# Optimization experiments

Hardware: AMD Instinct MI355X
Metric: run time of the kernel (lower is better)

## Reference

```python
import jax, jax.numpy as jnp
import numpy as np

N, K, D = 16384, 16, 16
TWO_PI = 2.0 * np.pi


def setup_inputs() -> dict:
    key = jax.random.key(0)
    k1, k2, k3, k4 = jax.random.split(key, 4)
    X = jax.random.normal(k1, (N, D), dtype=jnp.float32)
    mu = jax.random.normal(k2, (K, D), dtype=jnp.float32)
    L = jax.random.normal(k3, (K, D, D), dtype=jnp.float32)
    weights = jax.random.uniform(k4, (K,), dtype=jnp.float32)
    return {"X": X, "mu": mu, "L": L, "weights": weights, "it": 0}


def reference(X, mu, L, weights, it):
    # Covariance matrices A_k = tril(L_k) @ tril(L_k)^T + I  -> [K, D, D]
    Tl = jnp.tril(L)
    A = jnp.einsum('kab,kcb->kac', Tl, Tl) + jnp.eye(D, dtype=L.dtype)
    Sigma = jnp.linalg.inv(A)                                  # [K, D, D]

    # Gaussian product for all pairs (i, j):
    #   S_ij = inv(Sigma_i + Sigma_j), m_ij = S_ij (Sigma_i mu_i + Sigma_j mu_j)
    Ssum = Sigma[:, None] + Sigma[None, :]                     # [K, K, D, D]
    S = jnp.linalg.inv(Ssum)                                   # [K, K, D, D]
    rhs = jnp.einsum('kab,kb->ka', Sigma, mu)                  # Sigma_k mu_k
    m = jnp.einsum('ijab,ijb->ija', S, rhs[:, None] + rhs[None, :])  # [K, K, D]

    # Normalizer of the product Gaussian: z_ij = ((2pi)^D det(S_ij))^(-1/2)
    z = 1.0 / jnp.sqrt((TWO_PI ** D) * jnp.linalg.det(S))      # [K, K]
    P = jnp.linalg.inv(S)                                      # precision, [K, K, D, D]

    # Pair coefficient _product_z(i, j) (uses A as covariance here, as in source)
    Asum = A[:, None] + A[None, :]                             # [K, K, D, D]
    dmu = mu[:, None] - mu[None, :]                            # [K, K, D]
    q_mu = jnp.einsum('ijd,ijde,ije->ij', dmu, jnp.linalg.inv(Asum), dmu)
    pz = jnp.exp(-0.5 * q_mu) / jnp.sqrt(jnp.linalg.det(TWO_PI * Asum))

    # Mahalanobis distance of every sample to every pair mean: [N, K, K]
    diff = X[:, None, None, :] - m[None]                       # [N, K, K, D]
    quad = jnp.einsum('nijd,ijde,nije->nij', diff, P, diff)

    coef = pz * z * (weights[:, None] * weights[None, :])      # [K, K]
    pdf = jnp.einsum('ij,nij->n', coef, jnp.exp(-0.5 * quad))  # [N]
    return jnp.mean(jnp.log(pdf))
```

## Files before the change

kernel.cpp:

```cpp
#include <hip/hip_runtime.h>
#include <math.h>

#define NTOT 16384
#define KK 16
#define DD 16
#define NPAIR 136

#define WS_RHS   0
#define WS_WP    1024
#define WS_LCS   9792
#define WS_SIG   10336
#define WS_AF    26720
#define WS_PART  10336
#define WS_END   43104

#define LN2PI 1.8378770664093454836f

__global__ __launch_bounds__(256) void gm_pre(const float* __restrict__ mu,
                                              const float* __restrict__ L,
                                              char* __restrict__ wsb) {
  const int tid = threadIdx.x;
  const int k = tid >> 4;
  const int r = tid & 15;

  const float* Lk = L + k * DD * DD;
  float Lx[DD];
  #pragma unroll
  for (int b = 0; b < DD; b++) Lx[b] = (b <= r) ? Lk[r * DD + b] : 0.0f;

  float Ar[DD];
  #pragma unroll
  for (int c = 0; c < DD; c++) {
    float s = (r == c) ? 1.0f : 0.0f;
    #pragma unroll
    for (int b = 0; b <= c; b++)
      s = fmaf(Lx[b], __shfl(Lx[b], c, 16), s);
    Ar[c] = s;
  }
  {
    float* Aout = (float*)(wsb + WS_AF) + k * DD * DD;
    #pragma unroll
    for (int c = 0; c < DD; c++) Aout[r * DD + c] = Ar[c];
  }

  float Gr[DD];
  #pragma unroll
  for (int m = 0; m < DD; m++) Gr[m] = 0.0f;
  #pragma unroll
  for (int c = 0; c < DD; c++) {
    float u = Ar[c];
    #pragma unroll
    for (int m = 0; m < c; m++)
      u = fmaf(-Gr[m], __shfl(Gr[m], c, 16), u);
    float d = sqrtf(__shfl(u, c, 16));
    float val = (r == c) ? d : u / d;
    if (r >= c) Gr[c] = val;
  }

  float Wc[DD];
  #pragma unroll
  for (int m = 0; m < DD; m++) Wc[m] = 0.0f;
  #pragma unroll
  for (int rr = 0; rr < DD; rr++) {
    float s = (r == rr) ? 1.0f : 0.0f;
    #pragma unroll
    for (int m = 0; m < rr; m++)
      s = fmaf(-__shfl(Gr[m], rr, 16), Wc[m], s);
    Wc[rr] = s / __shfl(Gr[rr], rr, 16);
  }
  {
    float* Wout = (float*)(wsb + WS_WP) + k * 137;
    #pragma unroll
    for (int rr = 0; rr < DD; rr++)
      if (rr >= r) Wout[rr * (rr + 1) / 2 + r] = Wc[rr];
  }

  float Sig[DD];
  #pragma unroll
  for (int b = 0; b < DD; b++) {
    float s = 0.0f;
    #pragma unroll
    for (int rr = 0; rr < DD; rr++)
      s = fmaf(Wc[rr], __shfl(Wc[rr], b, 16), s);
    Sig[b] = s;
  }
  {
    float* Sout = (float*)(wsb + WS_SIG) + k * DD * DD;
    #pragma unroll
    for (int b = 0; b < DD; b++) Sout[r * DD + b] = Sig[b];
  }

  {
    float muv = mu[k * DD + r];
    float s = 0.0f;
    #pragma unroll
    for (int b = 0; b < DD; b++)
      s = fmaf(Sig[b], __shfl(muv, b, 16), s);
    ((float*)(wsb + WS_RHS))[k * DD + r] = s;
  }
}

__global__ __launch_bounds__(256) void gm_pair(const float* __restrict__ mu,
                                               const float* __restrict__ wts,
                                               char* __restrict__ wsb) {
  const int tid = threadIdx.x;
  const int g = (blockIdx.x << 4) + (tid >> 4);
  const int r = tid & 15;
  if (g >= NPAIR) return;
  int i = 0, rem = g;
  while (rem >= (KK - i)) { rem -= (KK - i); i++; }
  const int j = i + rem;

  const float* Sf = (const float*)(wsb + WS_SIG);
  const float* Af = (const float*)(wsb + WS_AF);
  const float* Rf = (const float*)(wsb + WS_RHS);

  float Mr[DD], Gr[DD];

  #pragma unroll
  for (int c = 0; c < DD; c++)
    Mr[c] = Sf[i * 256 + r * DD + c] + Sf[j * 256 + r * DD + c];

  float ldS = 0.0f, mydinv = 0.0f;
  #pragma unroll
  for (int m = 0; m < DD; m++) Gr[m] = 0.0f;
  #pragma unroll
  for (int c = 0; c < DD; c++) {
    float u = Mr[c];
    #pragma unroll
    for (int m = 0; m < c; m++)
      u = fmaf(-Gr[m], __shfl(Gr[m], c, 16), u);
    float d2 = __shfl(u, c, 16);
    ldS += __logf(d2);
    float d = sqrtf(d2);
    float dinv = 1.0f / d;
    if (r == c) mydinv = dinv;
    float val = (r == c) ? d : u * dinv;
    if (r >= c) Gr[c] = val;
  }
  float cq = 0.0f;
  {
    float acc = Rf[i * DD + r] + Rf[j * DD + r];
    #pragma unroll
    for (int m = 0; m < DD; m++) {
      float ym = __shfl(acc, m, 16) * __shfl(mydinv, m, 16);
      cq = fmaf(ym, ym, cq);
      if (r > m) acc = fmaf(-Gr[m], ym, acc);
    }
  }

  #pragma unroll
  for (int c = 0; c < DD; c++)
    Mr[c] = Af[i * 256 + r * DD + c] + Af[j * 256 + r * DD + c];

  float ldA = 0.0f, mydinvA = 0.0f;
  #pragma unroll
  for (int m = 0; m < DD; m++) Gr[m] = 0.0f;
  #pragma unroll
  for (int c = 0; c < DD; c++) {
    float u = Mr[c];
    #pragma unroll
    for (int m = 0; m < c; m++)
      u = fmaf(-Gr[m], __shfl(Gr[m], c, 16), u);
    float d2 = __shfl(u, c, 16);
    ldA += __logf(d2);
    float d = sqrtf(d2);
    float dinv = 1.0f / d;
    if (r == c) mydinvA = dinv;
    float val = (r == c) ? d : u * dinv;
    if (r >= c) Gr[c] = val;
  }
  float q = 0.0f;
  {
    float acc = mu[i * DD + r] - mu[j * DD + r];
    #pragma unroll
    for (int m = 0; m < DD; m++) {
      float ym = __shfl(acc, m, 16) * __shfl(mydinvA, m, 16);
      q = fmaf(ym, ym, q);
      if (r > m) acc = fmaf(-Gr[m], ym, acc);
    }
  }

  if (r == 0) {
    float lC = -0.5f * q - 0.5f * ldA + 0.5f * ldS - (float)DD * LN2PI
               + __logf(wts[i]) + __logf(wts[j]) - 0.5f * cq;
    if (i < j) lC += 0.69314718056f;
    ((float*)(wsb + WS_LCS))[g] = lC;
  }
}

__global__ __launch_bounds__(256) void gm_main(const float* __restrict__ X,
                                               char* __restrict__ wsb) {
  __shared__ float sW[KK * 137];
  __shared__ float sR[KK * 17];
  __shared__ float sLC[NPAIR];
  __shared__ unsigned char sIJ[NPAIR];
  __shared__ float sX[256];
  __shared__ float sE[16 * 17];
  __shared__ double sD[16];

  const int tid = threadIdx.x;
  const int s = tid >> 4;
  const int r = tid & 15;

  {
    const float* Wp = (const float*)(wsb + WS_WP);
    for (int idx = tid; idx < KK * 137; idx += 256) sW[idx] = Wp[idx];
    const float* Rf = (const float*)(wsb + WS_RHS);
    if (tid < 256) sR[(tid >> 4) * 17 + (tid & 15)] = Rf[tid];
    const float* lc = (const float*)(wsb + WS_LCS);
    if (tid < NPAIR) {
      sLC[tid] = lc[tid];
      int i = 0, rem = tid;
      while (rem >= (KK - i)) { rem -= (KK - i); i++; }
      sIJ[tid] = (unsigned char)((i << 4) | (i + rem));
    }
    if (tid < 64)
      ((float4*)sX)[tid] = ((const float4*)(X + (size_t)blockIdx.x * 256))[tid];
  }
  __syncthreads();

  float x[DD];
  {
    float4 b0 = ((const float4*)sX)[s * 4 + 0];
    float4 b1 = ((const float4*)sX)[s * 4 + 1];
    float4 b2 = ((const float4*)sX)[s * 4 + 2];
    float4 b3 = ((const float4*)sX)[s * 4 + 3];
    x[0]=b0.x; x[1]=b0.y; x[2]=b0.z; x[3]=b0.w;
    x[4]=b1.x; x[5]=b1.y; x[6]=b1.z; x[7]=b1.w;
    x[8]=b2.x; x[9]=b2.y; x[10]=b2.z; x[11]=b2.w;
    x[12]=b3.x; x[13]=b3.y; x[14]=b3.z; x[15]=b3.w;
  }

  {
    const float* Wk = &sW[r * 137];
    float g = 0.0f;
    #pragma unroll
    for (int rr = 0; rr < DD; rr++) {
      float y = 0.0f;
      #pragma unroll
      for (int c = 0; c <= rr; c++) y = fmaf(Wk[rr * (rr + 1) / 2 + c], x[c], y);
      g = fmaf(y, y, g);
    }
    float h = 0.0f;
    #pragma unroll
    for (int d = 0; d < DD; d++) h = fmaf(sR[r * 17 + d], x[d], h);
    sE[s * 17 + r] = fmaf(-0.5f, g, h);
  }
  __syncthreads();

  float val[9];
  float T = -3.0e38f;
  #pragma unroll
  for (int t = 0; t < 9; t++) {
    int p = t * 16 + r;
    if (t < 8 || r < 8) {
      int ij = sIJ[p];
      val[t] = sLC[p] + sE[s * 17 + (ij >> 4)] + sE[s * 17 + (ij & 15)];
    } else {
      val[t] = -3.0e38f;
    }
    T = fmaxf(T, val[t]);
  }
  #pragma unroll
  for (int w = 1; w < 16; w <<= 1) T = fmaxf(T, __shfl_xor(T, w, 16));

  float sum = 0.0f;
  #pragma unroll
  for (int t = 0; t < 9; t++) sum += __expf(val[t] - T);
  #pragma unroll
  for (int w = 1; w < 16; w <<= 1) sum += __shfl_xor(sum, w, 16);

  if (r == 0) sD[s] = (double)(T + __logf(sum));
  __syncthreads();
  if (tid == 0) {
    double acc = 0.0;
    #pragma unroll
    for (int m = 0; m < 16; m++) acc += sD[m];
    ((double*)(wsb + WS_PART))[blockIdx.x] = acc;
  }
}

__global__ __launch_bounds__(256) void gm_fin(const double* __restrict__ part,
                                              float* __restrict__ out) {
  int t = threadIdx.x;
  double v = part[t] + part[t + 256] + part[t + 512] + part[t + 768];
  #pragma unroll
  for (int off = 32; off > 0; off >>= 1) v += __shfl_down(v, off);
  __shared__ double r4[4];
  if ((t & 63) == 0) r4[t >> 6] = v;
  __syncthreads();
  if (t == 0) out[0] = (float)((r4[0] + r4[1] + r4[2] + r4[3]) * (1.0 / 16384.0));
}

extern "C" void kernel_launch(void* const* d_in, const int* in_sizes, int n_in,
                              void* d_out, int out_size, void* d_ws, size_t ws_size,
                              hipStream_t stream) {
  const float* X   = (const float*)d_in[0];
  const float* mu  = (const float*)d_in[1];
  const float* L   = (const float*)d_in[2];
  const float* wts = (const float*)d_in[3];
  char* wsb = (char*)d_ws;
  if (ws_size < WS_END) return;

  hipLaunchKernelGGL(gm_pre,  dim3(1), dim3(256), 0, stream, mu, L, wsb);
  hipLaunchKernelGGL(gm_pair, dim3(9), dim3(256), 0, stream, mu, wts, wsb);
  hipLaunchKernelGGL(gm_main, dim3(NTOT / 16), dim3(256), 0, stream, X, wsb);
  hipLaunchKernelGGL(gm_fin,  dim3(1), dim3(256), 0, stream,
                     (const double*)(wsb + WS_PART), (float*)d_out);
}
```

Baseline: 38.07 us.

## Fuse per-component and pair prep kernels, merge final reduction via atomics

Merges the per-component setup and pair-coefficient kernels into one 1024-thread block that keeps Sigma, A and rhs in shared memory instead of round-tripping through global workspace. The main kernel now processes two 256-sample tiles per block and performs the final reduction with a fixed-point 64-bit atomic accumulator plus a last-block counter, removing the separate finish kernel. This cuts the launch count from four to two. In exchange, the pair work runs on a single block, and the fixed-point conversion slightly quantizes the sum.

```diff
diff --git a/kernel.cpp b/kernel.cpp
--- a/kernel.cpp
+++ b/kernel.cpp
@@ -9,188 +9,190 @@
 #define WS_RHS   0
 #define WS_WP    1024
 #define WS_LCS   9792
-#define WS_SIG   10336
-#define WS_AF    26720
-#define WS_PART  10336
-#define WS_END   43104
+#define WS_ACC   10336
+#define WS_CNT   10344
+#define WS_END   10352
 
 #define LN2PI 1.8378770664093454836f
-
-__global__ __launch_bounds__(256) void gm_pre(const float* __restrict__ mu,
-                                              const float* __restrict__ L,
-                                              char* __restrict__ wsb) {
+#define FXSCALE 268435456.0
+
+__global__ __launch_bounds__(1024) void gm_prep(const float* __restrict__ mu,
+                                                const float* __restrict__ L,
+                                                const float* __restrict__ wts,
+                                                char* __restrict__ wsb) {
+  __shared__ float sSig[KK * 256];
+  __shared__ float sA[KK * 256];
+  __shared__ float sR[256];
+
   const int tid = threadIdx.x;
-  const int k = tid >> 4;
+  if (tid == 0) {
+    *(unsigned long long*)(wsb + WS_ACC) = 0ULL;
+    *(unsigned long long*)(wsb + WS_CNT) = 0ULL;
+  }
+
+  if (tid < 256) {
+    const int k = tid >> 4;
+    const int r = tid & 15;
+
+    const float* Lk = L + k * DD * DD;
+    float Lx[DD];
+    #pragma unroll
+    for (int b = 0; b < DD; b++) Lx[b] = (b <= r) ? Lk[r * DD + b] : 0.0f;
+
+    float Ar[DD];
+    #pragma unroll
+    for (int c = 0; c < DD; c++) {
+      float s = (r == c) ? 1.0f : 0.0f;
+      #pragma unroll
+      for (int b = 0; b <= c; b++)
+        s = fmaf(Lx[b], __shfl(Lx[b], c, 16), s);
+      Ar[c] = s;
+      sA[k * 256 + r * DD + c] = s;
+    }
+
+    float Gr[DD];
+    #pragma unroll
+    for (int m = 0; m < DD; m++) Gr[m] = 0.0f;
+    #pragma unroll
+    for (int c = 0; c < DD; c++) {
+      float u = Ar[c];
+      #pragma unroll
+      for (int m = 0; m < c; m++)
+        u = fmaf(-Gr[m], __shfl(Gr[m], c, 16), u);
+      float d = sqrtf(__shfl(u, c, 16));
+      float val = (r == c) ? d : u / d;
+      if (r >= c) Gr[c] = val;
+    }
+
+    float Wc[DD];
+    #pragma unroll
+    for (int m = 0; m < DD; m++) Wc[m] = 0.0f;
+    #pragma unroll
+    for (int rr = 0; rr < DD; rr++) {
+      float s = (r == rr) ? 1.0f : 0.0f;
+      #pragma unroll
+      for (int m = 0; m < rr; m++)
+        s = fmaf(-__shfl(Gr[m], rr, 16), Wc[m], s);
+      Wc[rr] = s / __shfl(Gr[rr], rr, 16);
+    }
+    {
+      float* Wout = (float*)(wsb + WS_WP) + k * 137;
+      #pragma unroll
+      for (int rr = 0; rr < DD; rr++)
+        if (rr >= r) Wout[rr * (rr + 1) / 2 + r] = Wc[rr];
+    }
+
+    float Sig[DD];
+    #pragma unroll
+    for (int b = 0; b < DD; b++) {
+      float s = 0.0f;
+      #pragma unroll
+      for (int rr = 0; rr < DD; rr++)
+        s = fmaf(Wc[rr], __shfl(Wc[rr], b, 16), s);
+      Sig[b] = s;
+      sSig[k * 256 + r * DD + b] = s;
+    }
+
+    {
+      float muv = mu[k * DD + r];
+      float s = 0.0f;
+      #pragma unroll
+      for (int b = 0; b < DD; b++)
+        s = fmaf(Sig[b], __shfl(muv, b, 16), s);
+      sR[k * DD + r] = s;
+      ((float*)(wsb + WS_RHS))[k * DD + r] = s;
+    }
+  }
+  __syncthreads();
+
+  const int g2 = tid >> 4;
   const int r = tid & 15;
 
-  const float* Lk = L + k * DD * DD;
-  float Lx[DD];
-  #pragma unroll
-  for (int b = 0; b < DD; b++) Lx[b] = (b <= r) ? Lk[r * DD + b] : 0.0f;
-
-  float Ar[DD];
-  #pragma unroll
-  for (int c = 0; c < DD; c++) {
-    float s = (r == c) ? 1.0f : 0.0f;
-    #pragma unroll
-    for (int b = 0; b <= c; b++)
-      s = fmaf(Lx[b], __shfl(Lx[b], c, 16), s);
-    Ar[c] = s;
-  }
-  {
-    float* Aout = (float*)(wsb + WS_AF) + k * DD * DD;
-    #pragma unroll
-    for (int c = 0; c < DD; c++) Aout[r * DD + c] = Ar[c];
-  }
-
-  float Gr[DD];
-  #pragma unroll
-  for (int m = 0; m < DD; m++) Gr[m] = 0.0f;
-  #pragma unroll
-  for (int c = 0; c < DD; c++) {
-    float u = Ar[c];
-    #pragma unroll
-    for (int m = 0; m < c; m++)
-      u = fmaf(-Gr[m], __shfl(Gr[m], c, 16), u);
-    float d = sqrtf(__shfl(u, c, 16));
-    float val = (r == c) ? d : u / d;
-    if (r >= c) Gr[c] = val;
-  }
-
-  float Wc[DD];
-  #pragma unroll
-  for (int m = 0; m < DD; m++) Wc[m] = 0.0f;
-  #pragma unroll
-  for (int rr = 0; rr < DD; rr++) {
-    float s = (r == rr) ? 1.0f : 0.0f;
-    #pragma unroll
-    for (int m = 0; m < rr; m++)
-      s = fmaf(-__shfl(Gr[m], rr, 16), Wc[m], s);
-    Wc[rr] = s / __shfl(Gr[rr], rr, 16);
-  }
-  {
-    float* Wout = (float*)(wsb + WS_WP) + k * 137;
-    #pragma unroll
-    for (int rr = 0; rr < DD; rr++)
-      if (rr >= r) Wout[rr * (rr + 1) / 2 + r] = Wc[rr];
-  }
-
-  float Sig[DD];
-  #pragma unroll
-  for (int b = 0; b < DD; b++) {
-    float s = 0.0f;
-    #pragma unroll
-    for (int rr = 0; rr < DD; rr++)
-      s = fmaf(Wc[rr], __shfl(Wc[rr], b, 16), s);
-    Sig[b] = s;
-  }
-  {
-    float* Sout = (float*)(wsb + WS_SIG) + k * DD * DD;
-    #pragma unroll
-    for (int b = 0; b < DD; b++) Sout[r * DD + b] = Sig[b];
-  }
-
-  {
-    float muv = mu[k * DD + r];
-    float s = 0.0f;
-    #pragma unroll
-    for (int b = 0; b < DD; b++)
-      s = fmaf(Sig[b], __shfl(muv, b, 16), s);
-    ((float*)(wsb + WS_RHS))[k * DD + r] = s;
+  for (int t = 0; t < 3; t++) {
+    const int p = g2 + (t << 6);
+    if (p >= NPAIR) break;
+    int i = 0, rem = p;
+    while (rem >= (KK - i)) { rem -= (KK - i); i++; }
+    const int j = i + rem;
+
+    float Mr[DD], Gr[DD];
+
+    #pragma unroll
+    for (int c = 0; c < DD; c++)
+      Mr[c] = sSig[i * 256 + r * DD + c] + sSig[j * 256 + r * DD + c];
+
+    float ldS = 0.0f, mydinv = 0.0f;
+    #pragma unroll
+    for (int m = 0; m < DD; m++) Gr[m] = 0.0f;
+    #pragma unroll
+    for (int c = 0; c < DD; c++) {
+      float u = Mr[c];
+      #pragma unroll
+      for (int m = 0; m < c; m++)
+        u = fmaf(-Gr[m], __shfl(Gr[m], c, 16), u);
+      float d2 = __shfl(u, c, 16);
+      ldS += __logf(d2);
+      float d = sqrtf(d2);
+      float dinv = 1.0f / d;
+      if (r == c) mydinv = dinv;
+      float val = (r == c) ? d : u * dinv;
+      if (r >= c) Gr[c] = val;
+    }
+    float cq = 0.0f;
+    {
+      float acc = sR[i * DD + r] + sR[j * DD + r];
+      #pragma unroll
+      for (int m = 0; m < DD; m++) {
+        float ym = __shfl(acc, m, 16) * __shfl(mydinv, m, 16);
+        cq = fmaf(ym, ym, cq);
+        if (r > m) acc = fmaf(-Gr[m], ym, acc);
+      }
+    }
+
+    #pragma unroll
+    for (int c = 0; c < DD; c++)
+      Mr[c] = sA[i * 256 + r * DD + c] + sA[j * 256 + r * DD + c];
+
+    float ldA = 0.0f, mydinvA = 0.0f;
+    #pragma unroll
+    for (int m = 0; m < DD; m++) Gr[m] = 0.0f;
+    #pragma unroll
+    for (int c = 0; c < DD; c++) {
+      float u = Mr[c];
+      #pragma unroll
+      for (int m = 0; m < c; m++)
+        u = fmaf(-Gr[m], __shfl(Gr[m], c, 16), u);
+      float d2 = __shfl(u, c, 16);
+      ldA += __logf(d2);
+      float d = sqrtf(d2);
+      float dinv = 1.0f / d;
+      if (r == c) mydinvA = dinv;
+      float val = (r == c) ? d : u * dinv;
+      if (r >= c) Gr[c] = val;
+    }
+    float q = 0.0f;
+    {
+      float acc = mu[i * DD + r] - mu[j * DD + r];
+      #pragma unroll
+      for (int m = 0; m < DD; m++) {
+        float ym = __shfl(acc, m, 16) * __shfl(mydinvA, m, 16);
+        q = fmaf(ym, ym, q);
+        if (r > m) acc = fmaf(-Gr[m], ym, acc);
+      }
+    }
+
+    if (r == 0) {
+      float lC = -0.5f * q - 0.5f * ldA + 0.5f * ldS - (float)DD * LN2PI
+                 + __logf(wts[i]) + __logf(wts[j]) - 0.5f * cq;
+      if (i < j) lC += 0.69314718056f;
+      ((float*)(wsb + WS_LCS))[p] = lC;
+    }
   }
 }
 
-__global__ __launch_bounds__(256) void gm_pair(const float* __restrict__ mu,
-                                               const float* __restrict__ wts,
-                                               char* __restrict__ wsb) {
-  const int tid = threadIdx.x;
-  const int g = (blockIdx.x << 4) + (tid >> 4);
-  const int r = tid & 15;
-  if (g >= NPAIR) return;
-  int i = 0, rem = g;
-  while (rem >= (KK - i)) { rem -= (KK - i); i++; }
-  const int j = i + rem;
-
-  const float* Sf = (const float*)(wsb + WS_SIG);
-  const float* Af = (const float*)(wsb + WS_AF);
-  const float* Rf = (const float*)(wsb + WS_RHS);
-
-  float Mr[DD], Gr[DD];
-
-  #pragma unroll
-  for (int c = 0; c < DD; c++)
-    Mr[c] = Sf[i * 256 + r * DD + c] + Sf[j * 256 + r * DD + c];
-
-  float ldS = 0.0f, mydinv = 0.0f;
-  #pragma unroll
-  for (int m = 0; m < DD; m++) Gr[m] = 0.0f;
-  #pragma unroll
-  for (int c = 0; c < DD; c++) {
-    float u = Mr[c];
-    #pragma unroll
-    for (int m = 0; m < c; m++)
-      u = fmaf(-Gr[m], __shfl(Gr[m], c, 16), u);
-    float d2 = __shfl(u, c, 16);
-    ldS += __logf(d2);
-    float d = sqrtf(d2);
-    float dinv = 1.0f / d;
-    if (r == c) mydinv = dinv;
-    float val = (r == c) ? d : u * dinv;
-    if (r >= c) Gr[c] = val;
-  }
-  float cq = 0.0f;
-  {
-    float acc = Rf[i * DD + r] + Rf[j * DD + r];
-    #pragma unroll
-    for (int m = 0; m < DD; m++) {
-      float ym = __shfl(acc, m, 16) * __shfl(mydinv, m, 16);
-      cq = fmaf(ym, ym, cq);
-      if (r > m) acc = fmaf(-Gr[m], ym, acc);
-    }
-  }
-
-  #pragma unroll
-  for (int c = 0; c < DD; c++)
-    Mr[c] = Af[i * 256 + r * DD + c] + Af[j * 256 + r * DD + c];
-
-  float ldA = 0.0f, mydinvA = 0.0f;
-  #pragma unroll
-  for (int m = 0; m < DD; m++) Gr[m] = 0.0f;
-  #pragma unroll
-  for (int c = 0; c < DD; c++) {
-    float u = Mr[c];
-    #pragma unroll
-    for (int m = 0; m < c; m++)
-      u = fmaf(-Gr[m], __shfl(Gr[m], c, 16), u);
-    float d2 = __shfl(u, c, 16);
-    ldA += __logf(d2);
-    float d = sqrtf(d2);
-    float dinv = 1.0f / d;
-    if (r == c) mydinvA = dinv;
-    float val = (r == c) ? d : u * dinv;
-    if (r >= c) Gr[c] = val;
-  }
-  float q = 0.0f;
-  {
-    float acc = mu[i * DD + r] - mu[j * DD + r];
-    #pragma unroll
-    for (int m = 0; m < DD; m++) {
-      float ym = __shfl(acc, m, 16) * __shfl(mydinvA, m, 16);
-      q = fmaf(ym, ym, q);
-      if (r > m) acc = fmaf(-Gr[m], ym, acc);
-    }
-  }
-
-  if (r == 0) {
-    float lC = -0.5f * q - 0.5f * ldA + 0.5f * ldS - (float)DD * LN2PI
-               + __logf(wts[i]) + __logf(wts[j]) - 0.5f * cq;
-    if (i < j) lC += 0.69314718056f;
-    ((float*)(wsb + WS_LCS))[g] = lC;
-  }
-}
-
-__global__ __launch_bounds__(256) void gm_main(const float* __restrict__ X,
-                                               char* __restrict__ wsb) {
+__global__ __launch_bounds__(256) void gm_all(const float* __restrict__ X,
+                                              char* __restrict__ wsb,
+                                              float* __restrict__ out) {
   __shared__ float sW[KK * 137];
   __shared__ float sR[KK * 17];
   __shared__ float sLC[NPAIR];
@@ -207,7 +209,7 @@
     const float* Wp = (const float*)(wsb + WS_WP);
     for (int idx = tid; idx < KK * 137; idx += 256) sW[idx] = Wp[idx];
     const float* Rf = (const float*)(wsb + WS_RHS);
-    if (tid < 256) sR[(tid >> 4) * 17 + (tid & 15)] = Rf[tid];
+    sR[s * 17 + r] = Rf[tid];
     const float* lc = (const float*)(wsb + WS_LCS);
     if (tid < NPAIR) {
       sLC[tid] = lc[tid];
@@ -215,82 +217,93 @@
       while (rem >= (KK - i)) { rem -= (KK - i); i++; }
       sIJ[tid] = (unsigned char)((i << 4) | (i + rem));
     }
+  }
+
+  double blockAcc = 0.0;
+
+  #pragma unroll
+  for (int tile = 0; tile < 2; tile++) {
+    __syncthreads();
     if (tid < 64)
-      ((float4*)sX)[tid] = ((const float4*)(X + (size_t)blockIdx.x * 256))[tid];
-  }
-  __syncthreads();
-
-  float x[DD];
-  {
-    float4 b0 = ((const float4*)sX)[s * 4 + 0];
-    float4 b1 = ((const float4*)sX)[s * 4 + 1];
-    float4 b2 = ((const float4*)sX)[s * 4 + 2];
-    float4 b3 = ((const float4*)sX)[s * 4 + 3];
-    x[0]=b0.x; x[1]=b0.y; x[2]=b0.z; x[3]=b0.w;
-    x[4]=b1.x; x[5]=b1.y; x[6]=b1.z; x[7]=b1.w;
-    x[8]=b2.x; x[9]=b2.y; x[10]=b2.z; x[11]=b2.w;
-    x[12]=b3.x; x[13]=b3.y; x[14]=b3.z; x[15]=b3.w;
-  }
-
-  {
-    const float* Wk = &sW[r * 137];
-    float g = 0.0f;
-    #pragma unroll
-    for (int rr = 0; rr < DD; rr++) {
-      float y = 0.0f;
-      #pragma unroll
-      for (int c = 0; c <= rr; c++) y = fmaf(Wk[rr * (rr + 1) / 2 + c], x[c], y);
-      g = fmaf(y, y, g);
-    }
-    float h = 0.0f;
-    #pragma unroll
-    for (int d = 0; d < DD; d++) h = fmaf(sR[r * 17 + d], x[d], h);
-    sE[s * 17 + r] = fmaf(-0.5f, g, h);
-  }
-  __syncthreads();
-
-  float val[9];
-  float T = -3.0e38f;
-  #pragma unroll
-  for (int t = 0; t < 9; t++) {
-    int p = t * 16 + r;
-    if (t < 8 || r < 8) {
-      int ij = sIJ[p];
-      val[t] = sLC[p] + sE[s * 17 + (ij >> 4)] + sE[s * 17 + (ij & 15)];
-    } else {
-      val[t] = -3.0e38f;
-    }
-    T = fmaxf(T, val[t]);
-  }
-  #pragma unroll
-  for (int w = 1; w < 16; w <<= 1) T = fmaxf(T, __shfl_xor(T, w, 16));
-
-  float sum = 0.0f;
-  #pragma unroll
-  for (int t = 0; t < 9; t++) sum += __expf(val[t] - T);
-  #pragma unroll
-  for (int w = 1; w < 16; w <<= 1) sum += __shfl_xor(sum, w, 16);
-
-  if (r == 0) sD[s] = (double)(T + __logf(sum));
-  __syncthreads();
+      ((float4*)sX)[tid] =
+        ((const float4*)(X + ((size_t)blockIdx.x * 2 + tile) * 256))[tid];
+    __syncthreads();
+
+    float x[DD];
+    {
+      float4 b0 = ((const float4*)sX)[s * 4 + 0];
+      float4 b1 = ((const float4*)sX)[s * 4 + 1];
+      float4 b2 = ((const float4*)sX)[s * 4 + 2];
+      float4 b3 = ((const float4*)sX)[s * 4 + 3];
+      x[0]=b0.x; x[1]=b0.y; x[2]=b0.z; x[3]=b0.w;
+      x[4]=b1.x; x[5]=b1.y; x[6]=b1.z; x[7]=b1.w;
+      x[8]=b2.x; x[9]=b2.y; x[10]=b2.z; x[11]=b2.w;
+      x[12]=b3.x; x[13]=b3.y; x[14]=b3.z; x[15]=b3.w;
+    }
+
+    {
+      const float* Wk = &sW[r * 137];
+      float g = 0.0f;
+      #pragma unroll
+      for (int rr = 0; rr < DD; rr++) {
+        float y = 0.0f;
+        #pragma unroll
+        for (int c = 0; c <= rr; c++) y = fmaf(Wk[rr * (rr + 1) / 2 + c], x[c], y);
+        g = fmaf(y, y, g);
+      }
+      float h = 0.0f;
+      #pragma unroll
+      for (int d = 0; d < DD; d++) h = fmaf(sR[r * 17 + d], x[d], h);
+      sE[s * 17 + r] = fmaf(-0.5f, g, h);
+    }
+    __syncthreads();
+
+    float val[9];
+    float T = -3.0e38f;
+    #pragma unroll
+    for (int t = 0; t < 9; t++) {
+      int p = t * 16 + r;
+      if (t < 8 || r < 8) {
+        int ij = sIJ[p];
+        val[t] = sLC[p] + sE[s * 17 + (ij >> 4)] + sE[s * 17 + (ij & 15)];
+      } else {
+        val[t] = -3.0e38f;
+      }
+      T = fmaxf(T, val[t]);
+    }
+    #pragma unroll
+    for (int w = 1; w < 16; w <<= 1) T = fmaxf(T, __shfl_xor(T, w, 16));
+
+    float sum = 0.0f;
+    #pragma unroll
+    for (int t = 0; t < 9; t++) sum += __expf(val[t] - T);
+    #pragma unroll
+    for (int w = 1; w < 16; w <<= 1) sum += __shfl_xor(sum, w, 16);
+
+    if (r == 0) sD[s] = (double)(T + __logf(sum));
+    __syncthreads();
+    if (tid == 0) {
+      double acc = 0.0;
+      #pragma unroll
+      for (int m = 0; m < 16; m++) acc += sD[m];
+      blockAcc += acc;
+    }
+  }
+
   if (tid == 0) {
-    double acc = 0.0;
-    #pragma unroll
-    for (int m = 0; m < 16; m++) acc += sD[m];
-    ((double*)(wsb + WS_PART))[blockIdx.x] = acc;
-  }
-}
-
-__global__ __launch_bounds__(256) void gm_fin(const double* __restrict__ part,
-                                              float* __restrict__ out) {
-  int t = threadIdx.x;
-  double v = part[t] + part[t + 256] + part[t + 512] + part[t + 768];
-  #pragma unroll
-  for (int off = 32; off > 0; off >>= 1) v += __shfl_down(v, off);
-  __shared__ double r4[4];
-  if ((t & 63) == 0) r4[t >> 6] = v;
-  __syncthreads();
-  if (t == 0) out[0] = (float)((r4[0] + r4[1] + r4[2] + r4[3]) * (1.0 / 16384.0));
+    double scaled = blockAcc * FXSCALE;
+    long long fx = (long long)(scaled + (scaled >= 0.0 ? 0.5 : -0.5));
+    unsigned long long* acc = (unsigned long long*)(wsb + WS_ACC);
+    unsigned long long* cnt = (unsigned long long*)(wsb + WS_CNT);
+    atomicAdd(acc, (unsigned long long)fx);
+    __threadfence();
+    unsigned long long old = atomicAdd(cnt, 1ULL);
+    if (old == (unsigned long long)(gridDim.x - 1)) {
+      __threadfence();
+      unsigned long long tot = atomicAdd(acc, 0ULL);
+      out[0] = (float)((double)(long long)tot * (1.0 / FXSCALE) * (1.0 / 16384.0));
+    }
+  }
 }
 
 extern "C" void kernel_launch(void* const* d_in, const int* in_sizes, int n_in,
@@ -303,9 +316,7 @@
   char* wsb = (char*)d_ws;
   if (ws_size < WS_END) return;
 
-  hipLaunchKernelGGL(gm_pre,  dim3(1), dim3(256), 0, stream, mu, L, wsb);
-  hipLaunchKernelGGL(gm_pair, dim3(9), dim3(256), 0, stream, mu, wts, wsb);
-  hipLaunchKernelGGL(gm_main, dim3(NTOT / 16), dim3(256), 0, stream, X, wsb);
-  hipLaunchKernelGGL(gm_fin,  dim3(1), dim3(256), 0, stream,
-                     (const double*)(wsb + WS_PART), (float*)d_out);
+  hipLaunchKernelGGL(gm_prep, dim3(1), dim3(1024), 0, stream, mu, L, wts, wsb);
+  hipLaunchKernelGGL(gm_all,  dim3(NTOT / 32), dim3(256), 0, stream, X, wsb,
+                     (float*)d_out);
 }
```

After: 82.53 us. 117% more time.

## Fuse per-component prep into pair kernel with redundant per-block recompute

Applied to the files above, without the earlier changes.

Merges the single-block precompute kernel and the pair kernel into one launch of nine blocks. Each block redundantly recomputes all 16 Cholesky factors, inverses and Sigma into shared memory, then handles its 16 pairs from there, so there is no global round trip and one fewer launch. The Cholesky is also rewritten as a right-looking update using rsqrt, and the triangular solve is shared via helpers. The cost is that every block repeats the per-component work, while block 0 alone writes the global outputs that the main kernel reads.

```diff
diff --git a/kernel.cpp b/kernel.cpp
--- a/kernel.cpp
+++ b/kernel.cpp
@@ -6,19 +6,56 @@
 #define DD 16
 #define NPAIR 136
 
+#define NPREP 9
+
 #define WS_RHS   0
 #define WS_WP    1024
 #define WS_LCS   9792
-#define WS_SIG   10336
-#define WS_AF    26720
 #define WS_PART  10336
-#define WS_END   43104
+#define WS_END   18528
 
 #define LN2PI 1.8378770664093454836f
 
-__global__ __launch_bounds__(256) void gm_pre(const float* __restrict__ mu,
-                                              const float* __restrict__ L,
-                                              char* __restrict__ wsb) {
+#define SROW 17
+#define SMAT (SROW * DD)
+
+__device__ __forceinline__ float chol16_rl(float* Mr, int r, float* dinvv) {
+  float ld = 0.0f;
+  #pragma unroll
+  for (int c = 0; c < DD; c++) {
+    float d2 = __shfl(Mr[c], c, 16);
+    ld += __logf(d2);
+    float dinv = rsqrtf(d2);
+    dinvv[c] = dinv;
+    float v = Mr[c] * dinv;
+    Mr[c] = v;
+    #pragma unroll
+    for (int c2 = c + 1; c2 < DD; c2++)
+      Mr[c2] = fmaf(-v, __shfl(v, c2, 16), Mr[c2]);
+  }
+  return ld;
+}
+
+__device__ __forceinline__ float solve16(const float* G, int r,
+                                         const float* dinvv, float b) {
+  float acc = b, qq = 0.0f;
+  #pragma unroll
+  for (int m = 0; m < DD; m++) {
+    float ym = __shfl(acc, m, 16) * dinvv[m];
+    qq = fmaf(ym, ym, qq);
+    if (r > m) acc = fmaf(-G[m], ym, acc);
+  }
+  return qq;
+}
+
+__global__ __launch_bounds__(256) void gm_prep(const float* __restrict__ mu,
+                                               const float* __restrict__ L,
+                                               const float* __restrict__ wts,
+                                               char* __restrict__ wsb) {
+  __shared__ float sSig[KK * SMAT];
+  __shared__ float sA[KK * SMAT];
+  __shared__ float sR[256];
+
   const int tid = threadIdx.x;
   const int k = tid >> 4;
   const int r = tid & 15;
@@ -36,39 +73,27 @@
     for (int b = 0; b <= c; b++)
       s = fmaf(Lx[b], __shfl(Lx[b], c, 16), s);
     Ar[c] = s;
-  }
-  {
-    float* Aout = (float*)(wsb + WS_AF) + k * DD * DD;
-    #pragma unroll
-    for (int c = 0; c < DD; c++) Aout[r * DD + c] = Ar[c];
-  }
-
-  float Gr[DD];
-  #pragma unroll
-  for (int m = 0; m < DD; m++) Gr[m] = 0.0f;
-  #pragma unroll
-  for (int c = 0; c < DD; c++) {
-    float u = Ar[c];
-    #pragma unroll
-    for (int m = 0; m < c; m++)
-      u = fmaf(-Gr[m], __shfl(Gr[m], c, 16), u);
-    float d = sqrtf(__shfl(u, c, 16));
-    float val = (r == c) ? d : u / d;
-    if (r >= c) Gr[c] = val;
-  }
+    sA[k * SMAT + r * SROW + c] = s;
+  }
+
+  float dinvv[DD];
+  chol16_rl(Ar, r, dinvv);
 
   float Wc[DD];
-  #pragma unroll
-  for (int m = 0; m < DD; m++) Wc[m] = 0.0f;
-  #pragma unroll
-  for (int rr = 0; rr < DD; rr++) {
-    float s = (r == rr) ? 1.0f : 0.0f;
-    #pragma unroll
-    for (int m = 0; m < rr; m++)
-      s = fmaf(-__shfl(Gr[m], rr, 16), Wc[m], s);
-    Wc[rr] = s / __shfl(Gr[rr], rr, 16);
-  }
-  {
+  {
+    float acc[DD];
+    #pragma unroll
+    for (int m = 0; m < DD; m++) acc[m] = (r == m) ? 1.0f : 0.0f;
+    #pragma unroll
+    for (int m = 0; m < DD; m++) {
+      float w = acc[m] * dinvv[m];
+      Wc[m] = w;
+      #pragma unroll
+      for (int rr = m + 1; rr < DD; rr++)
+        acc[rr] = fmaf(-__shfl(Ar[m], rr, 16), w, acc[rr]);
+    }
+  }
+  if (blockIdx.x == 0) {
     float* Wout = (float*)(wsb + WS_WP) + k * 137;
     #pragma unroll
     for (int rr = 0; rr < DD; rr++)
@@ -83,11 +108,7 @@
     for (int rr = 0; rr < DD; rr++)
       s = fmaf(Wc[rr], __shfl(Wc[rr], b, 16), s);
     Sig[b] = s;
-  }
-  {
-    float* Sout = (float*)(wsb + WS_SIG) + k * DD * DD;
-    #pragma unroll
-    for (int b = 0; b < DD; b++) Sout[r * DD + b] = Sig[b];
+    sSig[k * SMAT + r * SROW + b] = s;
   }
 
   {
@@ -96,96 +117,37 @@
     #pragma unroll
     for (int b = 0; b < DD; b++)
       s = fmaf(Sig[b], __shfl(muv, b, 16), s);
-    ((float*)(wsb + WS_RHS))[k * DD + r] = s;
-  }
-}
-
-__global__ __launch_bounds__(256) void gm_pair(const float* __restrict__ mu,
-                                               const float* __restrict__ wts,
-                                               char* __restrict__ wsb) {
-  const int tid = threadIdx.x;
-  const int g = (blockIdx.x << 4) + (tid >> 4);
-  const int r = tid & 15;
-  if (g >= NPAIR) return;
-  int i = 0, rem = g;
+    sR[k * DD + r] = s;
+    if (blockIdx.x == 0) ((float*)(wsb + WS_RHS))[k * DD + r] = s;
+  }
+  __syncthreads();
+
+  const int p = blockIdx.x * 16 + k;
+  if (p >= NPAIR) return;
+  int i = 0, rem = p;
   while (rem >= (KK - i)) { rem -= (KK - i); i++; }
   const int j = i + rem;
 
-  const float* Sf = (const float*)(wsb + WS_SIG);
-  const float* Af = (const float*)(wsb + WS_AF);
-  const float* Rf = (const float*)(wsb + WS_RHS);
-
-  float Mr[DD], Gr[DD];
+  float Mr[DD];
+  float dv[DD];
 
   #pragma unroll
   for (int c = 0; c < DD; c++)
-    Mr[c] = Sf[i * 256 + r * DD + c] + Sf[j * 256 + r * DD + c];
-
-  float ldS = 0.0f, mydinv = 0.0f;
-  #pragma unroll
-  for (int m = 0; m < DD; m++) Gr[m] = 0.0f;
-  #pragma unroll
-  for (int c = 0; c < DD; c++) {
-    float u = Mr[c];
-    #pragma unroll
-    for (int m = 0; m < c; m++)
-      u = fmaf(-Gr[m], __shfl(Gr[m], c, 16), u);
-    float d2 = __shfl(u, c, 16);
-    ldS += __logf(d2);
-    float d = sqrtf(d2);
-    float dinv = 1.0f / d;
-    if (r == c) mydinv = dinv;
-    float val = (r == c) ? d : u * dinv;
-    if (r >= c) Gr[c] = val;
-  }
-  float cq = 0.0f;
-  {
-    float acc = Rf[i * DD + r] + Rf[j * DD + r];
-    #pragma unroll
-    for (int m = 0; m < DD; m++) {
-      float ym = __shfl(acc, m, 16) * __shfl(mydinv, m, 16);
-      cq = fmaf(ym, ym, cq);
-      if (r > m) acc = fmaf(-Gr[m], ym, acc);
-    }
-  }
+    Mr[c] = sSig[i * SMAT + r * SROW + c] + sSig[j * SMAT + r * SROW + c];
+  float ldS = chol16_rl(Mr, r, dv);
+  float cq = solve16(Mr, r, dv, sR[i * DD + r] + sR[j * DD + r]);
 
   #pragma unroll
   for (int c = 0; c < DD; c++)
-    Mr[c] = Af[i * 256 + r * DD + c] + Af[j * 256 + r * DD + c];
-
-  float ldA = 0.0f, mydinvA = 0.0f;
-  #pragma unroll
-  for (int m = 0; m < DD; m++) Gr[m] = 0.0f;
-  #pragma unroll
-  for (int c = 0; c < DD; c++) {
-    float u = Mr[c];
-    #pragma unroll
-    for (int m = 0; m < c; m++)
-      u = fmaf(-Gr[m], __shfl(Gr[m], c, 16), u);
-    float d2 = __shfl(u, c, 16);
-    ldA += __logf(d2);
-    float d = sqrtf(d2);
-    float dinv = 1.0f / d;
-    if (r == c) mydinvA = dinv;
-    float val = (r == c) ? d : u * dinv;
-    if (r >= c) Gr[c] = val;
-  }
-  float q = 0.0f;
-  {
-    float acc = mu[i * DD + r] - mu[j * DD + r];
-    #pragma unroll
-    for (int m = 0; m < DD; m++) {
-      float ym = __shfl(acc, m, 16) * __shfl(mydinvA, m, 16);
-      q = fmaf(ym, ym, q);
-      if (r > m) acc = fmaf(-Gr[m], ym, acc);
-    }
-  }
+    Mr[c] = sA[i * SMAT + r * SROW + c] + sA[j * SMAT + r * SROW + c];
+  float ldA = chol16_rl(Mr, r, dv);
+  float q = solve16(Mr, r, dv, mu[i * DD + r] - mu[j * DD + r]);
 
   if (r == 0) {
     float lC = -0.5f * q - 0.5f * ldA + 0.5f * ldS - (float)DD * LN2PI
                + __logf(wts[i]) + __logf(wts[j]) - 0.5f * cq;
     if (i < j) lC += 0.69314718056f;
-    ((float*)(wsb + WS_LCS))[g] = lC;
+    ((float*)(wsb + WS_LCS))[p] = lC;
   }
 }
 
@@ -207,7 +169,7 @@
     const float* Wp = (const float*)(wsb + WS_WP);
     for (int idx = tid; idx < KK * 137; idx += 256) sW[idx] = Wp[idx];
     const float* Rf = (const float*)(wsb + WS_RHS);
-    if (tid < 256) sR[(tid >> 4) * 17 + (tid & 15)] = Rf[tid];
+    sR[s * 17 + r] = Rf[tid];
     const float* lc = (const float*)(wsb + WS_LCS);
     if (tid < NPAIR) {
       sLC[tid] = lc[tid];
@@ -303,8 +265,7 @@
   char* wsb = (char*)d_ws;
   if (ws_size < WS_END) return;
 
-  hipLaunchKernelGGL(gm_pre,  dim3(1), dim3(256), 0, stream, mu, L, wsb);
-  hipLaunchKernelGGL(gm_pair, dim3(9), dim3(256), 0, stream, mu, wts, wsb);
+  hipLaunchKernelGGL(gm_prep, dim3(NPREP), dim3(256), 0, stream, mu, L, wts, wsb);
   hipLaunchKernelGGL(gm_main, dim3(NTOT / 16), dim3(256), 0, stream, X, wsb);
   hipLaunchKernelGGL(gm_fin,  dim3(1), dim3(256), 0, stream,
                      (const double*)(wsb + WS_PART), (float*)d_out);
```

Measured after the change: 32.09 us. 15.7% less time.
